# Performance work log

Hardware: AMD Instinct MI355X
Metric: run time of the kernel (lower is better)

## Reference

```python
import math
import jax, jax.numpy as jnp
import numpy as np

B, L, K, D, H, C, P, VP = 2, 2048, 32, 64, 4, 64, 4, 8
POS_SCALE = 10.0
OUT_DIM = H * (D + C + VP * 4)  # 640
HW_INIT = 0.541324854612918


def _gather(nodes, idx):
    # nodes: [B, L, ...feat], idx: [B, L, K] -> [B, L, K, ...feat]
    return jax.vmap(lambda n, i: n[i])(nodes, idx)


def _frames(n, ca, c):
    # Gram-Schmidt rigid frame from N, CA, C (AlphaFold from_3_points)
    v1 = c - ca
    v2 = n - ca
    e1 = v1 / jnp.linalg.norm(v1, axis=-1, keepdims=True)
    u2 = v2 - e1 * jnp.sum(e1 * v2, axis=-1, keepdims=True)
    e2 = u2 / jnp.linalg.norm(u2, axis=-1, keepdims=True)
    e3 = jnp.cross(e1, e2)
    R = jnp.stack([e1, e2, e3], axis=-1)  # [B,L,3,3], columns e1,e2,e3
    return R, ca


def _ln(x, g, b, eps=1e-5):
    mu = x.mean(-1, keepdims=True)
    var = ((x - mu) ** 2).mean(-1, keepdims=True)
    return (x - mu) / jnp.sqrt(var + eps) * g + b


def setup_inputs() -> dict:
    key = jax.random.key(0)
    ks = jax.random.split(key, 16)
    w = lambda k, shp: jax.random.normal(k, shp, dtype=jnp.float32) * 0.02
    inp = {
        'h_V': jax.random.normal(ks[0], (B, L, D), dtype=jnp.float32),
        'h_E': jax.random.normal(ks[1], (B, L, K, D), dtype=jnp.float32),
        'E_idx': jax.random.randint(ks[2], (B, L, K), 0, L, dtype=jnp.int32),
        'X': jax.random.normal(ks[3], (B, L, 3, 3), dtype=jnp.float32),
        'mask_V': jnp.ones((B, L), dtype=jnp.float32),
        'mask_attend': jnp.ones((B, L, K), dtype=jnp.float32),
        'Wq': w(ks[4], (D, H * C)), 'bq': jnp.zeros((H * C,), jnp.float32),
        'Wkv': w(ks[5], (D, 2 * H * C)), 'bkv': jnp.zeros((2 * H * C,), jnp.float32),
        'Wqp': w(ks[6], (D, H * P * 3)), 'bqp': jnp.zeros((H * P * 3,), jnp.float32),
        'Wkvp': w(ks[7], (D, H * (P + VP) * 3)), 'bkvp': jnp.zeros((H * (P + VP) * 3,), jnp.float32),
        'Wb': w(ks[8], (D, H)), 'bb': jnp.zeros((H,), jnp.float32),
        'head_weights': jnp.full((H,), HW_INIT, dtype=jnp.float32),
        'Wout': w(ks[9], (OUT_DIM, D)), 'bout': jnp.zeros((D,), jnp.float32),
        'ln0_g': jnp.ones((D,), jnp.float32), 'ln0_b': jnp.zeros((D,), jnp.float32),
        'ln1_g': jnp.ones((D,), jnp.float32), 'ln1_b': jnp.zeros((D,), jnp.float32),
        'Wd1': w(ks[10], (D, 4 * D)), 'bd1': jnp.zeros((4 * D,), jnp.float32),
        'Wd2': w(ks[11], (4 * D, D)), 'bd2': jnp.zeros((D,), jnp.float32),
    }
    return inp


def reference(h_V, h_E, E_idx, X, mask_V, mask_attend,
              Wq, bq, Wkv, bkv, Wqp, bqp, Wkvp, bkvp, Wb, bb, head_weights,
              Wout, bout, ln0_g, ln0_b, ln1_g, ln1_b, Wd1, bd1, Wd2, bd2):
    sX = X / POS_SCALE
    R, t = _frames(sX[..., 0, :], sX[..., 1, :], sX[..., 2, :])

    q = (h_V @ Wq + bq).reshape(B, L, H, C)
    kv = (h_V @ Wkv + bkv).reshape(B, L, H, 2 * C)
    k, v = kv[..., :C], kv[..., C:]

    def frame_points(lin):
        p = jnp.stack(jnp.split(lin, 3, axis=-1), axis=-1)  # [B,L,n,3]
        return jnp.einsum('blij,blpj->blpi', R, p) + t[:, :, None, :]

    q_pts = frame_points(h_V @ Wqp + bqp).reshape(B, L, H, P, 3)
    kv_pts = frame_points(h_V @ Wkvp + bkvp).reshape(B, L, H, P + VP, 3)
    k_pts, v_pts = kv_pts[..., :P, :], kv_pts[..., P:, :]

    b = h_E @ Wb + bb  # [B,L,K,H]
    a = jnp.einsum('blhc,blkhc->blkh', q, _gather(k, E_idx)) * math.sqrt(1.0 / (3 * C))
    a = a + math.sqrt(1.0 / 3) * b

    d = q_pts[:, :, None] - _gather(k_pts, E_idx)  # [B,L,K,H,P,3]
    pt = jnp.sum(d * d, axis=-1)  # [B,L,K,H,P]
    hw = jax.nn.softplus(head_weights)
    pt = math.sqrt(1.0 / (3 * (P * 9.0 / 2))) * hw[None, None, None, :, None] * pt
    pt = -0.5 * jnp.sum(pt, axis=-1)  # [B,L,K,H]

    att_mask = 100000.0 * (mask_attend - 1.0)
    a = jax.nn.softmax(a + pt + att_mask[..., None], axis=-2)  # softmax over K

    o = jnp.einsum('blkh,blkhc->blhc', a, _gather(v, E_idx)).reshape(B, L, H * C)
    o_pt = jnp.einsum('blkh,blkhpx->blhpx', a, _gather(v_pts, E_idx))
    o_pt = jnp.einsum('blji,blhpj->blhpi', R, o_pt - t[:, :, None, None, :])  # invert_apply
    o_pt_norm = jnp.sqrt(jnp.sum(o_pt * o_pt, axis=-1) + 1e-8).reshape(B, L, H * VP)
    o_pt = o_pt.reshape(B, L, H * VP, 3)
    o_pair = jnp.einsum('blkh,blkc->blhc', a, h_E).reshape(B, L, H * D)

    s = jnp.concatenate([o, o_pt[..., 0], o_pt[..., 1], o_pt[..., 2], o_pt_norm, o_pair], axis=-1)
    s = s @ Wout + bout

    h = _ln(h_V + s, ln0_g, ln0_b)
    m = jax.nn.relu(h @ Wd1 + bd1) @ Wd2 + bd2
    h = _ln(h + m, ln1_g, ln1_b)
    return h * mask_V[..., None]
```

## Files before the change

kernel.cpp:

```cpp
#include <hip/hip_runtime.h>
#include <hip/hip_bf16.h>
#include <math.h>

#define L_ 2048
#define NN 4096

#define OFF_Q   0u
#define OFF_K   1048576u
#define OFF_V   2097152u
#define OFF_QP  3145728u
#define OFF_KP  3342336u
#define OFF_VP  3538944u
#define OFF_RT  3932160u
#define OFF_S   3981312u

__device__ __forceinline__ float wsum64(float x) {
#pragma unroll
  for (int o = 32; o > 0; o >>= 1) x += __shfl_xor(x, o, 64);
  return x;
}

__device__ __forceinline__ float bf_lo(unsigned u) { return __uint_as_float(u << 16); }
__device__ __forceinline__ float bf_hi(unsigned u) { return __uint_as_float(u & 0xffff0000u); }

__global__ __launch_bounds__(256) void k_proj(
    const float* __restrict__ hV, const float* __restrict__ X,
    const float* __restrict__ Wq, const float* __restrict__ bq,
    const float* __restrict__ Wkv, const float* __restrict__ bkv,
    const float* __restrict__ Wqp, const float* __restrict__ bqp,
    const float* __restrict__ Wkvp, const float* __restrict__ bkvp,
    float* __restrict__ ws)
{
  __shared__ __align__(16) float hv[16][64];
  __shared__ float lin[16][192];
  __shared__ float rt[16][12];
  const int tid = threadIdx.x;
  const int node0 = blockIdx.x * 16;
  *(float4*)&hv[tid >> 4][(tid & 15) * 4] = *(const float4*)&hV[(size_t)node0*64 + tid*4];
  __syncthreads();

  if (blockIdx.y < 3) {
    const int j = blockIdx.y * 256 + tid;
    const float* Wcol; int stride; float bias;
    if (j < 256) { Wcol = Wq + j; stride = 256; bias = bq[j]; }
    else { const int jj = j - 256; Wcol = Wkv + jj; stride = 512; bias = bkv[jj]; }

    float acc[16];
#pragma unroll
    for (int n = 0; n < 16; ++n) acc[n] = 0.f;
    for (int i = 0; i < 64; i += 4) {
      const float w0 = Wcol[(i+0)*stride];
      const float w1 = Wcol[(i+1)*stride];
      const float w2 = Wcol[(i+2)*stride];
      const float w3 = Wcol[(i+3)*stride];
#pragma unroll
      for (int n = 0; n < 16; ++n) {
        const float4 h4 = *(const float4*)&hv[n][i];
        acc[n] = fmaf(h4.x, w0, fmaf(h4.y, w1, fmaf(h4.z, w2, fmaf(h4.w, w3, acc[n]))));
      }
    }
    float* qf = ws + OFF_Q;
    __hip_bfloat16* kfb = (__hip_bfloat16*)(ws + OFF_K);
    __hip_bfloat16* vfb = (__hip_bfloat16*)(ws + OFF_V);
    if (j < 256) {
#pragma unroll
      for (int n = 0; n < 16; ++n) qf[(size_t)(node0+n)*256 + j] = acc[n] + bias;
    } else {
      const int jj = j - 256; const int h = jj >> 7; const int r = jj & 127;
      __hip_bfloat16* dst = (r < 64) ? (kfb + h*64 + r) : (vfb + h*64 + (r - 64));
#pragma unroll
      for (int n = 0; n < 16; ++n) dst[(size_t)(node0+n)*256] = __float2bfloat16(acc[n] + bias);
    }
    return;
  }

  if (tid < 192) {
    const float* Wcol; int stride; float bias;
    if (tid < 48) { Wcol = Wqp + tid; stride = 48; bias = bqp[tid]; }
    else { Wcol = Wkvp + (tid - 48); stride = 144; bias = bkvp[tid - 48]; }
    float acc[16];
#pragma unroll
    for (int n = 0; n < 16; ++n) acc[n] = 0.f;
    for (int i = 0; i < 64; i += 4) {
      const float w0 = Wcol[(i+0)*stride];
      const float w1 = Wcol[(i+1)*stride];
      const float w2 = Wcol[(i+2)*stride];
      const float w3 = Wcol[(i+3)*stride];
#pragma unroll
      for (int n = 0; n < 16; ++n) {
        const float4 h4 = *(const float4*)&hv[n][i];
        acc[n] = fmaf(h4.x, w0, fmaf(h4.y, w1, fmaf(h4.z, w2, fmaf(h4.w, w3, acc[n]))));
      }
    }
#pragma unroll
    for (int n = 0; n < 16; ++n) lin[n][tid] = acc[n] + bias;
  }
  float* rtw = ws + OFF_RT;
  if (tid < 16) {
    const float* x = X + (size_t)(node0 + tid) * 9;
    const float Nx=x[0]/10.f, Ny=x[1]/10.f, Nz=x[2]/10.f;
    const float Ax=x[3]/10.f, Ay=x[4]/10.f, Az=x[5]/10.f;
    const float Cx=x[6]/10.f, Cy=x[7]/10.f, Cz=x[8]/10.f;
    const float v1x=Cx-Ax, v1y=Cy-Ay, v1z=Cz-Az;
    const float v2x=Nx-Ax, v2y=Ny-Ay, v2z=Nz-Az;
    const float inv1 = 1.f/sqrtf(v1x*v1x+v1y*v1y+v1z*v1z);
    const float e1x=v1x*inv1, e1y=v1y*inv1, e1z=v1z*inv1;
    const float d12 = e1x*v2x+e1y*v2y+e1z*v2z;
    const float u2x=v2x-e1x*d12, u2y=v2y-e1y*d12, u2z=v2z-e1z*d12;
    const float inv2 = 1.f/sqrtf(u2x*u2x+u2y*u2y+u2z*u2z);
    const float e2x=u2x*inv2, e2y=u2y*inv2, e2z=u2z*inv2;
    const float e3x=e1y*e2z-e1z*e2y;
    const float e3y=e1z*e2x-e1x*e2z;
    const float e3z=e1x*e2y-e1y*e2x;
    const float r[12] = {e1x,e2x,e3x, e1y,e2y,e3y, e1z,e2z,e3z, Ax,Ay,Az};
#pragma unroll
    for (int q = 0; q < 12; ++q) { rt[tid][q] = r[q]; rtw[(size_t)(node0+tid)*12 + q] = r[q]; }
  }
  __syncthreads();
  float* qp = ws + OFF_QP;
  float* kp = ws + OFF_KP;
  float* vp = ws + OFF_VP;
  for (int item = tid; item < 1024; item += 256) {
    const int n = item >> 6, m = item & 63;
    const int node = node0 + n;
    float p0, p1, p2; float* dst;
    if (m < 16) {
      p0 = lin[n][m]; p1 = lin[n][16 + m]; p2 = lin[n][32 + m];
      dst = qp + (size_t)node*48 + m*3;
    } else {
      const int mm = m - 16;
      p0 = lin[n][48 + mm]; p1 = lin[n][96 + mm]; p2 = lin[n][144 + mm];
      const int h = mm / 12, pp = mm % 12;
      if (pp < 4) dst = kp + (size_t)node*48 + (h*4+pp)*3;
      else        dst = vp + (size_t)node*96 + (h*8+(pp-4))*3;
    }
    const float gx = rt[n][0]*p0 + rt[n][1]*p1 + rt[n][2]*p2 + rt[n][9];
    const float gy = rt[n][3]*p0 + rt[n][4]*p1 + rt[n][5]*p2 + rt[n][10];
    const float gz = rt[n][6]*p0 + rt[n][7]*p1 + rt[n][8]*p2 + rt[n][11];
    dst[0]=gx; dst[1]=gy; dst[2]=gz;
  }
}

__global__ __launch_bounds__(256) void k_attn(
    const float* __restrict__ hE, const int* __restrict__ Eidx,
    const float* __restrict__ maskAtt,
    const float* __restrict__ Wb, const float* __restrict__ bbv,
    const float* __restrict__ hwts,
    float* __restrict__ ws)
{
  __shared__ float sHE[32][65];
  __shared__ __align__(16) float sPV[32][100];
  __shared__ __align__(16) float sA[4][36];
  __shared__ float sWb[256];
  __shared__ __align__(16) float sQ[256];
  const int tid = threadIdx.x;
  const int rb = blockIdx.x & 7, qb = blockIdx.x >> 3;
  const int bat = rb >> 2;
  const int node = bat * L_ + (rb & 3) * 512 + qb;
  const int h = tid >> 6, lane = tid & 63;
  const int kk = lane >> 1, c2 = lane & 1;
  const float* qf  = ws + OFF_Q;
  const unsigned short* kfb = (const unsigned short*)(ws + OFF_K);
  const unsigned short* vfb = (const unsigned short*)(ws + OFF_V);
  const float* qpw = ws + OFF_QP;
  const float* kpw = ws + OFF_KP;
  const float* vpw = ws + OFF_VP;
  const float* rtw = ws + OFF_RT;
  float* sw = ws + OFF_S;

  int nbs[32];
#pragma unroll
  for (int u = 0; u < 32; ++u) nbs[u] = bat*L_ + Eidx[(size_t)node*32 + u];

  const float4* he4 = (const float4*)(hE + (size_t)node*2048);
  const float4 st0 = he4[tid], st1 = he4[tid + 256];
  float4 pst[3];
#pragma unroll
  for (int i = 0; i < 3; ++i) {
    const int idx = tid + 256*i;
    pst[i] = *(const float4*)(vpw + (size_t)nbs[idx/24]*96 + (idx%24)*4);
  }
  const float wbv = Wb[tid];
  const float qv  = qf[(size_t)node*256 + tid];

  unsigned short vvr[32];
#pragma unroll
  for (int u = 0; u < 32; ++u) vvr[u] = vfb[(size_t)nbs[u]*256 + tid];

  const int nb = nbs[kk];
  const float mval = maskAtt[(size_t)node*32 + kk];
  const uint4* krow4 = (const uint4*)(kfb + (size_t)nb*256 + h*64 + c2*32);
  const uint4 kb0 = krow4[0], kb1 = krow4[1], kb2 = krow4[2], kb3 = krow4[3];
  const float* kpr = kpw + (size_t)nb*48 + h*12 + c2*6;
  const float2 kp0 = *(const float2*)&kpr[0];
  const float2 kp1 = *(const float2*)&kpr[2];
  const float2 kp2 = *(const float2*)&kpr[4];

  {
    const int r0 = tid >> 4, c0 = (tid & 15) * 4;
    sHE[r0][c0] = st0.x; sHE[r0][c0+1] = st0.y; sHE[r0][c0+2] = st0.z; sHE[r0][c0+3] = st0.w;
    const int r1 = (tid + 256) >> 4, c1 = ((tid + 256) & 15) * 4;
    sHE[r1][c1] = st1.x; sHE[r1][c1+1] = st1.y; sHE[r1][c1+2] = st1.z; sHE[r1][c1+3] = st1.w;
#pragma unroll
    for (int i = 0; i < 3; ++i) {
      const int idx = tid + 256*i;
      *(float4*)&sPV[idx/24][(idx%24)*4] = pst[i];
    }
    sWb[tid] = wbv;
    sQ[tid] = qv;
  }
  __syncthreads();

  float bt = 0.f;
  {
    const float* wbp = &sWb[c2*128 + h];
#pragma unroll
    for (int i = 0; i < 32; ++i)
      bt = fmaf(sHE[kk][c2*32 + i], wbp[i*4], bt);
  }

  float dot = 0.f;
  {
    const float4* q4 = (const float4*)&sQ[h*64 + c2*32];
    const float4 qa0 = q4[0], qa1 = q4[1], qa2 = q4[2], qa3 = q4[3];
    const float4 qa4 = q4[4], qa5 = q4[5], qa6 = q4[6], qa7 = q4[7];
    dot = fmaf(qa0.x, bf_lo(kb0.x), dot); dot = fmaf(qa0.y, bf_hi(kb0.x), dot);
    dot = fmaf(qa0.z, bf_lo(kb0.y), dot); dot = fmaf(qa0.w, bf_hi(kb0.y), dot);
    dot = fmaf(qa1.x, bf_lo(kb0.z), dot); dot = fmaf(qa1.y, bf_hi(kb0.z), dot);
    dot = fmaf(qa1.z, bf_lo(kb0.w), dot); dot = fmaf(qa1.w, bf_hi(kb0.w), dot);
    dot = fmaf(qa2.x, bf_lo(kb1.x), dot); dot = fmaf(qa2.y, bf_hi(kb1.x), dot);
    dot = fmaf(qa2.z, bf_lo(kb1.y), dot); dot = fmaf(qa2.w, bf_hi(kb1.y), dot);
    dot = fmaf(qa3.x, bf_lo(kb1.z), dot); dot = fmaf(qa3.y, bf_hi(kb1.z), dot);
    dot = fmaf(qa3.z, bf_lo(kb1.w), dot); dot = fmaf(qa3.w, bf_hi(kb1.w), dot);
    dot = fmaf(qa4.x, bf_lo(kb2.x), dot); dot = fmaf(qa4.y, bf_hi(kb2.x), dot);
    dot = fmaf(qa4.z, bf_lo(kb2.y), dot); dot = fmaf(qa4.w, bf_hi(kb2.y), dot);
    dot = fmaf(qa5.x, bf_lo(kb2.z), dot); dot = fmaf(qa5.y, bf_hi(kb2.z), dot);
    dot = fmaf(qa5.z, bf_lo(kb2.w), dot); dot = fmaf(qa5.w, bf_hi(kb2.w), dot);
    dot = fmaf(qa6.x, bf_lo(kb3.x), dot); dot = fmaf(qa6.y, bf_hi(kb3.x), dot);
    dot = fmaf(qa6.z, bf_lo(kb3.y), dot); dot = fmaf(qa6.w, bf_hi(kb3.y), dot);
    dot = fmaf(qa7.x, bf_lo(kb3.z), dot); dot = fmaf(qa7.y, bf_hi(kb3.z), dot);
    dot = fmaf(qa7.z, bf_lo(kb3.w), dot); dot = fmaf(qa7.w, bf_hi(kb3.w), dot);
  }

  float pt = 0.f;
  {
    const float* qpr = qpw + (size_t)node*48 + h*12 + c2*6;
    const float2 qp0 = *(const float2*)&qpr[0];
    const float2 qp1 = *(const float2*)&qpr[2];
    const float2 qp2 = *(const float2*)&qpr[4];
    float d0 = qp0.x - kp0.x, d1 = qp0.y - kp0.y;
    pt = fmaf(d0, d0, fmaf(d1, d1, pt));
    d0 = qp1.x - kp1.x; d1 = qp1.y - kp1.y;
    pt = fmaf(d0, d0, fmaf(d1, d1, pt));
    d0 = qp2.x - kp2.x; d1 = qp2.y - kp2.y;
    pt = fmaf(d0, d0, fmaf(d1, d1, pt));
  }

  {
    dot += __shfl_xor(dot, 1, 64);
    bt  += __shfl_xor(bt, 1, 64);
    pt  += __shfl_xor(pt, 1, 64);
    const float hw = log1pf(expf(hwts[h]));
    const float lg = 0.07216878364870322f*dot
                   + 0.5773502691896258f*(bt + bbv[h])
                   - 0.06804138174397717f*hw*pt
                   + 100000.f*(mval - 1.f);
    float m = lg;
#pragma unroll
    for (int o = 2; o <= 32; o <<= 1) m = fmaxf(m, __shfl_xor(m, o, 64));
    const float e = __expf(lg - m);
    float ssum = e;
#pragma unroll
    for (int o = 2; o <= 32; o <<= 1) ssum += __shfl_xor(ssum, o, 64);
    if (c2 == 0) sA[h][kk] = e / ssum;
  }

  const int t24 = lane % 24;
  const int pcol = h*24 + t24;
  float o0 = 0.f, o1 = 0.f, op0 = 0.f, op1 = 0.f, g0 = 0.f, g1 = 0.f;
#pragma unroll
  for (int u = 0; u < 32; u += 4) {
    const float4 a4 = *(const float4*)&sA[h][u];
    o0  = fmaf(a4.x, __uint_as_float((unsigned)vvr[u] << 16), o0);
    o1  = fmaf(a4.y, __uint_as_float((unsigned)vvr[u+1] << 16), o1);
    op0 = fmaf(a4.x, sHE[u][lane], op0);
    op1 = fmaf(a4.y, sHE[u+1][lane], op1);
    g0  = fmaf(a4.x, sPV[u][pcol], g0);
    g1  = fmaf(a4.y, sPV[u+1][pcol], g1);
    o0  = fmaf(a4.z, __uint_as_float((unsigned)vvr[u+2] << 16), o0);
    o1  = fmaf(a4.w, __uint_as_float((unsigned)vvr[u+3] << 16), o1);
    op0 = fmaf(a4.z, sHE[u+2][lane], op0);
    op1 = fmaf(a4.w, sHE[u+3][lane], op1);
    g0  = fmaf(a4.z, sPV[u+2][pcol], g0);
    g1  = fmaf(a4.w, sPV[u+3][pcol], g1);
  }
  const float o = o0 + o1, op = op0 + op1, g = g0 + g1;
  float* srow = sw + (size_t)node*640;
  srow[tid] = o;
  srow[384 + tid] = op;

  const int p = lane & 7;
  const float gx = __shfl(g, 3*p,   64);
  const float gy = __shfl(g, 3*p+1, 64);
  const float gz = __shfl(g, 3*p+2, 64);
  if (lane < 8) {
    const float* rt = rtw + (size_t)node*12;
    const float dx = gx - rt[9], dy = gy - rt[10], dz = gz - rt[11];
    const float l0 = rt[0]*dx + rt[3]*dy + rt[6]*dz;
    const float l1 = rt[1]*dx + rt[4]*dy + rt[7]*dz;
    const float l2 = rt[2]*dx + rt[5]*dy + rt[8]*dz;
    const int o8 = h*8 + p;
    srow[256 + o8] = l0;
    srow[288 + o8] = l1;
    srow[320 + o8] = l2;
    srow[352 + o8] = sqrtf(fmaf(l0,l0,fmaf(l1,l1,l2*l2)) + 1e-8f);
  }
}

__global__ __launch_bounds__(256) void k_tail(
    const float* __restrict__ hV, const float* __restrict__ maskV,
    const float* __restrict__ Wout, const float* __restrict__ bout,
    const float* __restrict__ ln0g, const float* __restrict__ ln0b,
    const float* __restrict__ Wd1, const float* __restrict__ bd1,
    const float* __restrict__ Wd2, const float* __restrict__ bd2,
    const float* __restrict__ ln1g, const float* __restrict__ ln1b,
    const float* __restrict__ ws, float* __restrict__ out)
{
  __shared__ __align__(16) float sS[4][640];
  __shared__ float sPart[4][4][64];
  __shared__ float sH0[4][64];
  __shared__ float sHid[4][256];
  __shared__ float sY[4][64];
  const int tid = threadIdx.x;
  const int w = tid >> 6, lane = tid & 63;
  const int node0 = blockIdx.x * 4;
  const float* sw = ws + OFF_S;
  for (int idx = tid; idx < 640; idx += 256)
    *(float4*)&(&sS[0][0])[idx*4] = *(const float4*)&sw[(size_t)node0*640 + idx*4];
  __syncthreads();
  {
    float acc[4];
#pragma unroll
    for (int n = 0; n < 4; ++n) acc[n] = 0.f;
    for (int i = w*160; i < w*160+160; ++i) {
      const float wv = Wout[i*64 + lane];
#pragma unroll
      for (int n = 0; n < 4; ++n) acc[n] = fmaf(sS[n][i], wv, acc[n]);
    }
#pragma unroll
    for (int n = 0; n < 4; ++n) sPart[w][n][lane] = acc[n];
  }
  __syncthreads();
  {
    const int n = tid >> 6, j = tid & 63;
    const float u = sPart[0][n][j] + sPart[1][n][j] + sPart[2][n][j] + sPart[3][n][j];
    sH0[n][j] = u + bout[j] + hV[(size_t)(node0+n)*64 + j];
  }
  __syncthreads();
  {
    const int n = w;
    const float x = sH0[n][lane];
    const float mu = wsum64(x) * 0.015625f;
    const float dv = x - mu;
    const float var = wsum64(dv*dv) * 0.015625f;
    sH0[n][lane] = dv * rsqrtf(var + 1e-5f) * ln0g[lane] + ln0b[lane];
  }
  __syncthreads();
  {
    float acc[4];
#pragma unroll
    for (int n = 0; n < 4; ++n) acc[n] = 0.f;
    for (int i = 0; i < 64; ++i) {
      const float wv = Wd1[i*256 + tid];
#pragma unroll
      for (int n = 0; n < 4; ++n) acc[n] = fmaf(sH0[n][i], wv, acc[n]);
    }
    const float b1 = bd1[tid];
#pragma unroll
    for (int n = 0; n < 4; ++n) sHid[n][tid] = fmaxf(acc[n] + b1, 0.f);
  }
  __syncthreads();
  {
    float acc[4];
#pragma unroll
    for (int n = 0; n < 4; ++n) acc[n] = 0.f;
    for (int i = w*64; i < w*64+64; ++i) {
      const float wv = Wd2[i*64 + lane];
#pragma unroll
      for (int n = 0; n < 4; ++n) acc[n] = fmaf(sHid[n][i], wv, acc[n]);
    }
#pragma unroll
    for (int n = 0; n < 4; ++n) sPart[w][n][lane] = acc[n];
  }
  __syncthreads();
  {
    const int n = tid >> 6, j = tid & 63;
    const float u = sPart[0][n][j] + sPart[1][n][j] + sPart[2][n][j] + sPart[3][n][j];
    sY[n][j] = u + bd2[j] + sH0[n][j];
  }
  __syncthreads();
  {
    const int n = w;
    const float x = sY[n][lane];
    const float mu = wsum64(x) * 0.015625f;
    const float dv = x - mu;
    const float var = wsum64(dv*dv) * 0.015625f;
    const float hv1 = dv * rsqrtf(var + 1e-5f) * ln1g[lane] + ln1b[lane];
    out[(size_t)(node0+n)*64 + lane] = hv1 * maskV[node0 + n];
  }
}

extern "C" void kernel_launch(void* const* d_in, const int* in_sizes, int n_in,
                              void* d_out, int out_size, void* d_ws, size_t ws_size,
                              hipStream_t stream)
{
  const float* hV   = (const float*)d_in[0];
  const float* hE   = (const float*)d_in[1];
  const int*   Eidx = (const int*)  d_in[2];
  const float* X    = (const float*)d_in[3];
  const float* maskV= (const float*)d_in[4];
  const float* maskA= (const float*)d_in[5];
  const float* Wq   = (const float*)d_in[6];
  const float* bq   = (const float*)d_in[7];
  const float* Wkv  = (const float*)d_in[8];
  const float* bkv  = (const float*)d_in[9];
  const float* Wqp  = (const float*)d_in[10];
  const float* bqp  = (const float*)d_in[11];
  const float* Wkvp = (const float*)d_in[12];
  const float* bkvp = (const float*)d_in[13];
  const float* Wb   = (const float*)d_in[14];
  const float* bbv  = (const float*)d_in[15];
  const float* hwts = (const float*)d_in[16];
  const float* Wout = (const float*)d_in[17];
  const float* bout = (const float*)d_in[18];
  const float* ln0g = (const float*)d_in[19];
  const float* ln0b = (const float*)d_in[20];
  const float* ln1g = (const float*)d_in[21];
  const float* ln1b = (const float*)d_in[22];
  const float* Wd1  = (const float*)d_in[23];
  const float* bd1  = (const float*)d_in[24];
  const float* Wd2  = (const float*)d_in[25];
  const float* bd2  = (const float*)d_in[26];
  float* ws = (float*)d_ws;
  float* out = (float*)d_out;

  k_proj<<<dim3(256, 4), 256, 0, stream>>>(hV, X, Wq, bq, Wkv, bkv,
                                           Wqp, bqp, Wkvp, bkvp, ws);
  k_attn<<<4096, 256, 0, stream>>>(hE, Eidx, maskA, Wb, bbv, hwts, ws);
  k_tail<<<1024, 256, 0, stream>>>(hV, maskV, Wout, bout, ln0g, ln0b,
                                   Wd1, bd1, Wd2, bd2, ln1g, ln1b, ws, out);
}
```

Before: 71.21 us.

## Fuse attention and output MLP tail into one kernel over four nodes per block

Merges the attention kernel and the tail kernel (output projection, two layernorms and the MLP) into a single kernel. Each block now loops over four nodes, computes their attention outputs and keeps the concatenated feature rows in shared memory rather than writing them to a global workspace and reading them back. This removes one kernel launch and the global round trip of the intermediate feature rows. In exchange there are four times fewer blocks, the per-node gathers run one after another inside a block, and the shared-memory footprint grows, which may cut latency hiding and occupancy.

```diff
diff --git a/kernel.cpp b/kernel.cpp
--- a/kernel.cpp
+++ b/kernel.cpp
@@ -12,7 +12,6 @@
 #define OFF_KP  3342336u
 #define OFF_VP  3538944u
 #define OFF_RT  3932160u
-#define OFF_S   3981312u
 
 __device__ __forceinline__ float wsum64(float x) {
 #pragma unroll
@@ -141,22 +140,31 @@
   }
 }
 
-__global__ __launch_bounds__(256) void k_attn(
+__global__ __launch_bounds__(256) void k_fused(
     const float* __restrict__ hE, const int* __restrict__ Eidx,
     const float* __restrict__ maskAtt,
     const float* __restrict__ Wb, const float* __restrict__ bbv,
     const float* __restrict__ hwts,
-    float* __restrict__ ws)
+    const float* __restrict__ hV, const float* __restrict__ maskV,
+    const float* __restrict__ Wout, const float* __restrict__ bout,
+    const float* __restrict__ ln0g, const float* __restrict__ ln0b,
+    const float* __restrict__ Wd1, const float* __restrict__ bd1,
+    const float* __restrict__ Wd2, const float* __restrict__ bd2,
+    const float* __restrict__ ln1g, const float* __restrict__ ln1b,
+    const float* __restrict__ ws, float* __restrict__ out)
 {
-  __shared__ float sHE[32][65];
-  __shared__ __align__(16) float sPV[32][100];
-  __shared__ __align__(16) float sA[4][36];
-  __shared__ float sWb[256];
-  __shared__ __align__(16) float sQ[256];
+  __shared__ __align__(16) float sS[4][640];
+  __shared__ __align__(16) float sBuf[5936];
+  float (*sHE)[65]  = (float(*)[65]) sBuf;
+  float (*sPV)[100] = (float(*)[100])(sBuf + 2080);
+  float (*sA)[36]   = (float(*)[36]) (sBuf + 5280);
+  float* sWb        = sBuf + 5424;
+  float* sQ         = sBuf + 5680;
+
   const int tid = threadIdx.x;
   const int rb = blockIdx.x & 7, qb = blockIdx.x >> 3;
   const int bat = rb >> 2;
-  const int node = bat * L_ + (rb & 3) * 512 + qb;
+  const int node0 = bat * L_ + (rb & 3) * 512 + qb * 4;
   const int h = tid >> 6, lane = tid & 63;
   const int kk = lane >> 1, c2 = lane & 1;
   const float* qf  = ws + OFF_Q;
@@ -166,204 +174,192 @@
   const float* kpw = ws + OFF_KP;
   const float* vpw = ws + OFF_VP;
   const float* rtw = ws + OFF_RT;
-  float* sw = ws + OFF_S;
-
-  int nbs[32];
-#pragma unroll
-  for (int u = 0; u < 32; ++u) nbs[u] = bat*L_ + Eidx[(size_t)node*32 + u];
-
-  const float4* he4 = (const float4*)(hE + (size_t)node*2048);
-  const float4 st0 = he4[tid], st1 = he4[tid + 256];
-  float4 pst[3];
-#pragma unroll
-  for (int i = 0; i < 3; ++i) {
-    const int idx = tid + 256*i;
-    pst[i] = *(const float4*)(vpw + (size_t)nbs[idx/24]*96 + (idx%24)*4);
-  }
+
   const float wbv = Wb[tid];
-  const float qv  = qf[(size_t)node*256 + tid];
-
-  unsigned short vvr[32];
-#pragma unroll
-  for (int u = 0; u < 32; ++u) vvr[u] = vfb[(size_t)nbs[u]*256 + tid];
-
-  const int nb = nbs[kk];
-  const float mval = maskAtt[(size_t)node*32 + kk];
-  const uint4* krow4 = (const uint4*)(kfb + (size_t)nb*256 + h*64 + c2*32);
-  const uint4 kb0 = krow4[0], kb1 = krow4[1], kb2 = krow4[2], kb3 = krow4[3];
-  const float* kpr = kpw + (size_t)nb*48 + h*12 + c2*6;
-  const float2 kp0 = *(const float2*)&kpr[0];
-  const float2 kp1 = *(const float2*)&kpr[2];
-  const float2 kp2 = *(const float2*)&kpr[4];
-
-  {
-    const int r0 = tid >> 4, c0 = (tid & 15) * 4;
-    sHE[r0][c0] = st0.x; sHE[r0][c0+1] = st0.y; sHE[r0][c0+2] = st0.z; sHE[r0][c0+3] = st0.w;
-    const int r1 = (tid + 256) >> 4, c1 = ((tid + 256) & 15) * 4;
-    sHE[r1][c1] = st1.x; sHE[r1][c1+1] = st1.y; sHE[r1][c1+2] = st1.z; sHE[r1][c1+3] = st1.w;
+  const float hw  = log1pf(expf(hwts[h]));
+  const float bb  = bbv[h];
+
+  for (int nn = 0; nn < 4; ++nn) {
+    const int node = node0 + nn;
+    int nbs[32];
+#pragma unroll
+    for (int u = 0; u < 32; ++u) nbs[u] = bat*L_ + Eidx[(size_t)node*32 + u];
+
+    const float4* he4 = (const float4*)(hE + (size_t)node*2048);
+    const float4 st0 = he4[tid], st1 = he4[tid + 256];
+    float4 pst[3];
 #pragma unroll
     for (int i = 0; i < 3; ++i) {
       const int idx = tid + 256*i;
-      *(float4*)&sPV[idx/24][(idx%24)*4] = pst[i];
-    }
-    sWb[tid] = wbv;
-    sQ[tid] = qv;
-  }
-  __syncthreads();
-
-  float bt = 0.f;
-  {
-    const float* wbp = &sWb[c2*128 + h];
-#pragma unroll
-    for (int i = 0; i < 32; ++i)
-      bt = fmaf(sHE[kk][c2*32 + i], wbp[i*4], bt);
-  }
-
-  float dot = 0.f;
-  {
-    const float4* q4 = (const float4*)&sQ[h*64 + c2*32];
-    const float4 qa0 = q4[0], qa1 = q4[1], qa2 = q4[2], qa3 = q4[3];
-    const float4 qa4 = q4[4], qa5 = q4[5], qa6 = q4[6], qa7 = q4[7];
-    dot = fmaf(qa0.x, bf_lo(kb0.x), dot); dot = fmaf(qa0.y, bf_hi(kb0.x), dot);
-    dot = fmaf(qa0.z, bf_lo(kb0.y), dot); dot = fmaf(qa0.w, bf_hi(kb0.y), dot);
-    dot = fmaf(qa1.x, bf_lo(kb0.z), dot); dot = fmaf(qa1.y, bf_hi(kb0.z), dot);
-    dot = fmaf(qa1.z, bf_lo(kb0.w), dot); dot = fmaf(qa1.w, bf_hi(kb0.w), dot);
-    dot = fmaf(qa2.x, bf_lo(kb1.x), dot); dot = fmaf(qa2.y, bf_hi(kb1.x), dot);
-    dot = fmaf(qa2.z, bf_lo(kb1.y), dot); dot = fmaf(qa2.w, bf_hi(kb1.y), dot);
-    dot = fmaf(qa3.x, bf_lo(kb1.z), dot); dot = fmaf(qa3.y, bf_hi(kb1.z), dot);
-    dot = fmaf(qa3.z, bf_lo(kb1.w), dot); dot = fmaf(qa3.w, bf_hi(kb1.w), dot);
-    dot = fmaf(qa4.x, bf_lo(kb2.x), dot); dot = fmaf(qa4.y, bf_hi(kb2.x), dot);
-    dot = fmaf(qa4.z, bf_lo(kb2.y), dot); dot = fmaf(qa4.w, bf_hi(kb2.y), dot);
-    dot = fmaf(qa5.x, bf_lo(kb2.z), dot); dot = fmaf(qa5.y, bf_hi(kb2.z), dot);
-    dot = fmaf(qa5.z, bf_lo(kb2.w), dot); dot = fmaf(qa5.w, bf_hi(kb2.w), dot);
-    dot = fmaf(qa6.x, bf_lo(kb3.x), dot); dot = fmaf(qa6.y, bf_hi(kb3.x), dot);
-    dot = fmaf(qa6.z, bf_lo(kb3.y), dot); dot = fmaf(qa6.w, bf_hi(kb3.y), dot);
-    dot = fmaf(qa7.x, bf_lo(kb3.z), dot); dot = fmaf(qa7.y, bf_hi(kb3.z), dot);
-    dot = fmaf(qa7.z, bf_lo(kb3.w), dot); dot = fmaf(qa7.w, bf_hi(kb3.w), dot);
-  }
-
-  float pt = 0.f;
-  {
-    const float* qpr = qpw + (size_t)node*48 + h*12 + c2*6;
-    const float2 qp0 = *(const float2*)&qpr[0];
-    const float2 qp1 = *(const float2*)&qpr[2];
-    const float2 qp2 = *(const float2*)&qpr[4];
-    float d0 = qp0.x - kp0.x, d1 = qp0.y - kp0.y;
-    pt = fmaf(d0, d0, fmaf(d1, d1, pt));
-    d0 = qp1.x - kp1.x; d1 = qp1.y - kp1.y;
-    pt = fmaf(d0, d0, fmaf(d1, d1, pt));
-    d0 = qp2.x - kp2.x; d1 = qp2.y - kp2.y;
-    pt = fmaf(d0, d0, fmaf(d1, d1, pt));
-  }
-
-  {
-    dot += __shfl_xor(dot, 1, 64);
-    bt  += __shfl_xor(bt, 1, 64);
-    pt  += __shfl_xor(pt, 1, 64);
-    const float hw = log1pf(expf(hwts[h]));
-    const float lg = 0.07216878364870322f*dot
-                   + 0.5773502691896258f*(bt + bbv[h])
-                   - 0.06804138174397717f*hw*pt
-                   + 100000.f*(mval - 1.f);
-    float m = lg;
-#pragma unroll
-    for (int o = 2; o <= 32; o <<= 1) m = fmaxf(m, __shfl_xor(m, o, 64));
-    const float e = __expf(lg - m);
-    float ssum = e;
-#pragma unroll
-    for (int o = 2; o <= 32; o <<= 1) ssum += __shfl_xor(ssum, o, 64);
-    if (c2 == 0) sA[h][kk] = e / ssum;
-  }
-
-  const int t24 = lane % 24;
-  const int pcol = h*24 + t24;
-  float o0 = 0.f, o1 = 0.f, op0 = 0.f, op1 = 0.f, g0 = 0.f, g1 = 0.f;
-#pragma unroll
-  for (int u = 0; u < 32; u += 4) {
-    const float4 a4 = *(const float4*)&sA[h][u];
-    o0  = fmaf(a4.x, __uint_as_float((unsigned)vvr[u] << 16), o0);
-    o1  = fmaf(a4.y, __uint_as_float((unsigned)vvr[u+1] << 16), o1);
-    op0 = fmaf(a4.x, sHE[u][lane], op0);
-    op1 = fmaf(a4.y, sHE[u+1][lane], op1);
-    g0  = fmaf(a4.x, sPV[u][pcol], g0);
-    g1  = fmaf(a4.y, sPV[u+1][pcol], g1);
-    o0  = fmaf(a4.z, __uint_as_float((unsigned)vvr[u+2] << 16), o0);
-    o1  = fmaf(a4.w, __uint_as_float((unsigned)vvr[u+3] << 16), o1);
-    op0 = fmaf(a4.z, sHE[u+2][lane], op0);
-    op1 = fmaf(a4.w, sHE[u+3][lane], op1);
-    g0  = fmaf(a4.z, sPV[u+2][pcol], g0);
-    g1  = fmaf(a4.w, sPV[u+3][pcol], g1);
-  }
-  const float o = o0 + o1, op = op0 + op1, g = g0 + g1;
-  float* srow = sw + (size_t)node*640;
-  srow[tid] = o;
-  srow[384 + tid] = op;
-
-  const int p = lane & 7;
-  const float gx = __shfl(g, 3*p,   64);
-  const float gy = __shfl(g, 3*p+1, 64);
-  const float gz = __shfl(g, 3*p+2, 64);
-  if (lane < 8) {
-    const float* rt = rtw + (size_t)node*12;
-    const float dx = gx - rt[9], dy = gy - rt[10], dz = gz - rt[11];
-    const float l0 = rt[0]*dx + rt[3]*dy + rt[6]*dz;
-    const float l1 = rt[1]*dx + rt[4]*dy + rt[7]*dz;
-    const float l2 = rt[2]*dx + rt[5]*dy + rt[8]*dz;
-    const int o8 = h*8 + p;
-    srow[256 + o8] = l0;
-    srow[288 + o8] = l1;
-    srow[320 + o8] = l2;
-    srow[352 + o8] = sqrtf(fmaf(l0,l0,fmaf(l1,l1,l2*l2)) + 1e-8f);
-  }
-}
-
-__global__ __launch_bounds__(256) void k_tail(
-    const float* __restrict__ hV, const float* __restrict__ maskV,
-    const float* __restrict__ Wout, const float* __restrict__ bout,
-    const float* __restrict__ ln0g, const float* __restrict__ ln0b,
-    const float* __restrict__ Wd1, const float* __restrict__ bd1,
-    const float* __restrict__ Wd2, const float* __restrict__ bd2,
-    const float* __restrict__ ln1g, const float* __restrict__ ln1b,
-    const float* __restrict__ ws, float* __restrict__ out)
-{
-  __shared__ __align__(16) float sS[4][640];
-  __shared__ float sPart[4][4][64];
-  __shared__ float sH0[4][64];
-  __shared__ float sHid[4][256];
-  __shared__ float sY[4][64];
-  const int tid = threadIdx.x;
-  const int w = tid >> 6, lane = tid & 63;
-  const int node0 = blockIdx.x * 4;
-  const float* sw = ws + OFF_S;
-  for (int idx = tid; idx < 640; idx += 256)
-    *(float4*)&(&sS[0][0])[idx*4] = *(const float4*)&sw[(size_t)node0*640 + idx*4];
-  __syncthreads();
+      pst[i] = *(const float4*)(vpw + (size_t)nbs[idx/24]*96 + (idx%24)*4);
+    }
+    const float qv = qf[(size_t)node*256 + tid];
+
+    unsigned short vvr[32];
+#pragma unroll
+    for (int u = 0; u < 32; ++u) vvr[u] = vfb[(size_t)nbs[u]*256 + tid];
+
+    const int nb = nbs[kk];
+    const float mval = maskAtt[(size_t)node*32 + kk];
+    const uint4* krow4 = (const uint4*)(kfb + (size_t)nb*256 + h*64 + c2*32);
+    const uint4 kb0 = krow4[0], kb1 = krow4[1], kb2 = krow4[2], kb3 = krow4[3];
+    const float* kpr = kpw + (size_t)nb*48 + h*12 + c2*6;
+    const float2 kp0 = *(const float2*)&kpr[0];
+    const float2 kp1 = *(const float2*)&kpr[2];
+    const float2 kp2 = *(const float2*)&kpr[4];
+
+    __syncthreads();
+    {
+      const int r0 = tid >> 4, c0 = (tid & 15) * 4;
+      sHE[r0][c0] = st0.x; sHE[r0][c0+1] = st0.y; sHE[r0][c0+2] = st0.z; sHE[r0][c0+3] = st0.w;
+      const int r1 = (tid + 256) >> 4, c1 = ((tid + 256) & 15) * 4;
+      sHE[r1][c1] = st1.x; sHE[r1][c1+1] = st1.y; sHE[r1][c1+2] = st1.z; sHE[r1][c1+3] = st1.w;
+#pragma unroll
+      for (int i = 0; i < 3; ++i) {
+        const int idx = tid + 256*i;
+        *(float4*)&sPV[idx/24][(idx%24)*4] = pst[i];
+      }
+      sQ[tid] = qv;
+      if (nn == 0) sWb[tid] = wbv;
+    }
+    __syncthreads();
+
+    float bt = 0.f;
+    {
+      const float* wbp = &sWb[c2*128 + h];
+#pragma unroll
+      for (int i = 0; i < 32; ++i)
+        bt = fmaf(sHE[kk][c2*32 + i], wbp[i*4], bt);
+    }
+
+    float dot = 0.f;
+    {
+      const float4* q4 = (const float4*)&sQ[h*64 + c2*32];
+      const float4 qa0 = q4[0], qa1 = q4[1], qa2 = q4[2], qa3 = q4[3];
+      const float4 qa4 = q4[4], qa5 = q4[5], qa6 = q4[6], qa7 = q4[7];
+      dot = fmaf(qa0.x, bf_lo(kb0.x), dot); dot = fmaf(qa0.y, bf_hi(kb0.x), dot);
+      dot = fmaf(qa0.z, bf_lo(kb0.y), dot); dot = fmaf(qa0.w, bf_hi(kb0.y), dot);
+      dot = fmaf(qa1.x, bf_lo(kb0.z), dot); dot = fmaf(qa1.y, bf_hi(kb0.z), dot);
+      dot = fmaf(qa1.z, bf_lo(kb0.w), dot); dot = fmaf(qa1.w, bf_hi(kb0.w), dot);
+      dot = fmaf(qa2.x, bf_lo(kb1.x), dot); dot = fmaf(qa2.y, bf_hi(kb1.x), dot);
+      dot = fmaf(qa2.z, bf_lo(kb1.y), dot); dot = fmaf(qa2.w, bf_hi(kb1.y), dot);
+      dot = fmaf(qa3.x, bf_lo(kb1.z), dot); dot = fmaf(qa3.y, bf_hi(kb1.z), dot);
+      dot = fmaf(qa3.z, bf_lo(kb1.w), dot); dot = fmaf(qa3.w, bf_hi(kb1.w), dot);
+      dot = fmaf(qa4.x, bf_lo(kb2.x), dot); dot = fmaf(qa4.y, bf_hi(kb2.x), dot);
+      dot = fmaf(qa4.z, bf_lo(kb2.y), dot); dot = fmaf(qa4.w, bf_hi(kb2.y), dot);
+      dot = fmaf(qa5.x, bf_lo(kb2.z), dot); dot = fmaf(qa5.y, bf_hi(kb2.z), dot);
+      dot = fmaf(qa5.z, bf_lo(kb2.w), dot); dot = fmaf(qa5.w, bf_hi(kb2.w), dot);
+      dot = fmaf(qa6.x, bf_lo(kb3.x), dot); dot = fmaf(qa6.y, bf_hi(kb3.x), dot);
+      dot = fmaf(qa6.z, bf_lo(kb3.y), dot); dot = fmaf(qa6.w, bf_hi(kb3.y), dot);
+      dot = fmaf(qa7.x, bf_lo(kb3.z), dot); dot = fmaf(qa7.y, bf_hi(kb3.z), dot);
+      dot = fmaf(qa7.z, bf_lo(kb3.w), dot); dot = fmaf(qa7.w, bf_hi(kb3.w), dot);
+    }
+
+    float pt = 0.f;
+    {
+      const float* qpr = qpw + (size_t)node*48 + h*12 + c2*6;
+      const float2 qp0 = *(const float2*)&qpr[0];
+      const float2 qp1 = *(const float2*)&qpr[2];
+      const float2 qp2 = *(const float2*)&qpr[4];
+      float d0 = qp0.x - kp0.x, d1 = qp0.y - kp0.y;
+      pt = fmaf(d0, d0, fmaf(d1, d1, pt));
+      d0 = qp1.x - kp1.x; d1 = qp1.y - kp1.y;
+      pt = fmaf(d0, d0, fmaf(d1, d1, pt));
+      d0 = qp2.x - kp2.x; d1 = qp2.y - kp2.y;
+      pt = fmaf(d0, d0, fmaf(d1, d1, pt));
+    }
+
+    {
+      dot += __shfl_xor(dot, 1, 64);
+      bt  += __shfl_xor(bt, 1, 64);
+      pt  += __shfl_xor(pt, 1, 64);
+      const float lg = 0.07216878364870322f*dot
+                     + 0.5773502691896258f*(bt + bb)
+                     - 0.06804138174397717f*hw*pt
+                     + 100000.f*(mval - 1.f);
+      float m = lg;
+#pragma unroll
+      for (int o = 2; o <= 32; o <<= 1) m = fmaxf(m, __shfl_xor(m, o, 64));
+      const float e = __expf(lg - m);
+      float ssum = e;
+#pragma unroll
+      for (int o = 2; o <= 32; o <<= 1) ssum += __shfl_xor(ssum, o, 64);
+      if (c2 == 0) sA[h][kk] = e / ssum;
+    }
+
+    const int t24 = lane % 24;
+    const int pcol = h*24 + t24;
+    float o0 = 0.f, o1 = 0.f, op0 = 0.f, op1 = 0.f, g0 = 0.f, g1 = 0.f;
+#pragma unroll
+    for (int u = 0; u < 32; u += 4) {
+      const float4 a4 = *(const float4*)&sA[h][u];
+      o0  = fmaf(a4.x, __uint_as_float((unsigned)vvr[u] << 16), o0);
+      o1  = fmaf(a4.y, __uint_as_float((unsigned)vvr[u+1] << 16), o1);
+      op0 = fmaf(a4.x, sHE[u][lane], op0);
+      op1 = fmaf(a4.y, sHE[u+1][lane], op1);
+      g0  = fmaf(a4.x, sPV[u][pcol], g0);
+      g1  = fmaf(a4.y, sPV[u+1][pcol], g1);
+      o0  = fmaf(a4.z, __uint_as_float((unsigned)vvr[u+2] << 16), o0);
+      o1  = fmaf(a4.w, __uint_as_float((unsigned)vvr[u+3] << 16), o1);
+      op0 = fmaf(a4.z, sHE[u+2][lane], op0);
+      op1 = fmaf(a4.w, sHE[u+3][lane], op1);
+      g0  = fmaf(a4.z, sPV[u+2][pcol], g0);
+      g1  = fmaf(a4.w, sPV[u+3][pcol], g1);
+    }
+    sS[nn][tid] = o0 + o1;
+    sS[nn][384 + tid] = op0 + op1;
+    const float g = g0 + g1;
+
+    const int p = lane & 7;
+    const float gx = __shfl(g, 3*p,   64);
+    const float gy = __shfl(g, 3*p+1, 64);
+    const float gz = __shfl(g, 3*p+2, 64);
+    if (lane < 8) {
+      const float* rt = rtw + (size_t)node*12;
+      const float dx = gx - rt[9], dy = gy - rt[10], dz = gz - rt[11];
+      const float l0 = rt[0]*dx + rt[3]*dy + rt[6]*dz;
+      const float l1 = rt[1]*dx + rt[4]*dy + rt[7]*dz;
+      const float l2 = rt[2]*dx + rt[5]*dy + rt[8]*dz;
+      const int o8 = h*8 + p;
+      sS[nn][256 + o8] = l0;
+      sS[nn][288 + o8] = l1;
+      sS[nn][320 + o8] = l2;
+      sS[nn][352 + o8] = sqrtf(fmaf(l0,l0,fmaf(l1,l1,l2*l2)) + 1e-8f);
+    }
+  }
+  __syncthreads();
+
+  float (*tPart)[4][64] = (float(*)[4][64]) sBuf;
+  float (*tH0)[64]  = (float(*)[64]) (sBuf + 1024);
+  float (*tHid)[256]= (float(*)[256])(sBuf + 1280);
+  float (*tY)[64]   = (float(*)[64]) (sBuf + 2304);
+  const int w = h, jlane = lane;
+
   {
     float acc[4];
 #pragma unroll
     for (int n = 0; n < 4; ++n) acc[n] = 0.f;
     for (int i = w*160; i < w*160+160; ++i) {
-      const float wv = Wout[i*64 + lane];
+      const float wv = Wout[i*64 + jlane];
 #pragma unroll
       for (int n = 0; n < 4; ++n) acc[n] = fmaf(sS[n][i], wv, acc[n]);
     }
 #pragma unroll
-    for (int n = 0; n < 4; ++n) sPart[w][n][lane] = acc[n];
+    for (int n = 0; n < 4; ++n) tPart[w][n][jlane] = acc[n];
   }
   __syncthreads();
   {
     const int n = tid >> 6, j = tid & 63;
-    const float u = sPart[0][n][j] + sPart[1][n][j] + sPart[2][n][j] + sPart[3][n][j];
-    sH0[n][j] = u + bout[j] + hV[(size_t)(node0+n)*64 + j];
-  }
-  __syncthreads();
-  {
-    const int n = w;
-    const float x = sH0[n][lane];
+    const float u = tPart[0][n][j] + tPart[1][n][j] + tPart[2][n][j] + tPart[3][n][j];
+    tH0[n][j] = u + bout[j] + hV[(size_t)(node0+n)*64 + j];
+  }
+  __syncthreads();
+  {
+    const float x = tH0[w][jlane];
     const float mu = wsum64(x) * 0.015625f;
     const float dv = x - mu;
     const float var = wsum64(dv*dv) * 0.015625f;
-    sH0[n][lane] = dv * rsqrtf(var + 1e-5f) * ln0g[lane] + ln0b[lane];
+    tH0[w][jlane] = dv * rsqrtf(var + 1e-5f) * ln0g[jlane] + ln0b[jlane];
   }
   __syncthreads();
   {
@@ -373,11 +369,11 @@
     for (int i = 0; i < 64; ++i) {
       const float wv = Wd1[i*256 + tid];
 #pragma unroll
-      for (int n = 0; n < 4; ++n) acc[n] = fmaf(sH0[n][i], wv, acc[n]);
+      for (int n = 0; n < 4; ++n) acc[n] = fmaf(tH0[n][i], wv, acc[n]);
     }
     const float b1 = bd1[tid];
 #pragma unroll
-    for (int n = 0; n < 4; ++n) sHid[n][tid] = fmaxf(acc[n] + b1, 0.f);
+    for (int n = 0; n < 4; ++n) tHid[n][tid] = fmaxf(acc[n] + b1, 0.f);
   }
   __syncthreads();
   {
@@ -385,28 +381,27 @@
 #pragma unroll
     for (int n = 0; n < 4; ++n) acc[n] = 0.f;
     for (int i = w*64; i < w*64+64; ++i) {
-      const float wv = Wd2[i*64 + lane];
-#pragma unroll
-      for (int n = 0; n < 4; ++n) acc[n] = fmaf(sHid[n][i], wv, acc[n]);
-    }
-#pragma unroll
-    for (int n = 0; n < 4; ++n) sPart[w][n][lane] = acc[n];
+      const float wv = Wd2[i*64 + jlane];
+#pragma unroll
+      for (int n = 0; n < 4; ++n) acc[n] = fmaf(tHid[n][i], wv, acc[n]);
+    }
+#pragma unroll
+    for (int n = 0; n < 4; ++n) tPart[w][n][jlane] = acc[n];
   }
   __syncthreads();
   {
     const int n = tid >> 6, j = tid & 63;
-    const float u = sPart[0][n][j] + sPart[1][n][j] + sPart[2][n][j] + sPart[3][n][j];
-    sY[n][j] = u + bd2[j] + sH0[n][j];
-  }
-  __syncthreads();
-  {
-    const int n = w;
-    const float x = sY[n][lane];
+    const float u = tPart[0][n][j] + tPart[1][n][j] + tPart[2][n][j] + tPart[3][n][j];
+    tY[n][j] = u + bd2[j] + tH0[n][j];
+  }
+  __syncthreads();
+  {
+    const float x = tY[w][jlane];
     const float mu = wsum64(x) * 0.015625f;
     const float dv = x - mu;
     const float var = wsum64(dv*dv) * 0.015625f;
-    const float hv1 = dv * rsqrtf(var + 1e-5f) * ln1g[lane] + ln1b[lane];
-    out[(size_t)(node0+n)*64 + lane] = hv1 * maskV[node0 + n];
+    const float hv1 = dv * rsqrtf(var + 1e-5f) * ln1g[jlane] + ln1b[jlane];
+    out[(size_t)(node0+w)*64 + jlane] = hv1 * maskV[node0 + w];
   }
 }
 
@@ -446,7 +441,7 @@
 
   k_proj<<<dim3(256, 4), 256, 0, stream>>>(hV, X, Wq, bq, Wkv, bkv,
                                            Wqp, bqp, Wkvp, bkvp, ws);
-  k_attn<<<4096, 256, 0, stream>>>(hE, Eidx, maskA, Wb, bbv, hwts, ws);
-  k_tail<<<1024, 256, 0, stream>>>(hV, maskV, Wout, bout, ln0g, ln0b,
-                                   Wd1, bd1, Wd2, bd2, ln1g, ln1b, ws, out);
+  k_fused<<<1024, 256, 0, stream>>>(hE, Eidx, maskA, Wb, bbv, hwts,
+                                    hV, maskV, Wout, bout, ln0g, ln0b,
+                                    Wd1, bd1, Wd2, bd2, ln1g, ln1b, ws, out);
 }
```

Measured after the change: 100.3 us. +40.8%, slower.
